# Optimization experiments

Hardware: AMD Instinct MI355X
Metric: run time of the kernel (lower is better)

Reference implementation:

```python
import jax, jax.numpy as jnp
import numpy as np

B, T, D, H = 256, 512, 128, 512

_PARAM_NAMES = [
    "W_i", "U_i", "b_i", "W_i_p", "U_i_p", "b_i_p", "W_i_n", "U_i_n", "b_i_n",
    "W_f", "U_f", "b_f", "W_c", "U_c", "b_c", "W_c_p", "U_c_p", "b_c_p",
    "W_c_n", "U_c_n", "b_c_n", "W_o", "U_o", "b_o", "W_a", "b_a",
]

def _param_shape(name):
    if name == "W_a":
        return (H, H)
    if name.startswith("W"):
        return (D, H)
    if name.startswith("U"):
        return (H, H)
    return (H,)

def setup_inputs() -> dict:
    key = jax.random.key(0)
    keys = jax.random.split(key, len(_PARAM_NAMES) + 3)
    stdv = 1.0 / np.sqrt(H)
    out = {}
    for i, name in enumerate(_PARAM_NAMES):
        out[name] = jax.random.uniform(keys[i], _param_shape(name), jnp.float32, -stdv, stdv)
    out["Y"] = jax.random.normal(keys[-3], (B, T, D), jnp.float32)
    out["P"] = jax.random.normal(keys[-2], (B, T, D), jnp.float32)
    out["N"] = jax.random.normal(keys[-1], (B, T, D), jnp.float32)
    return out


def reference(Y, P, N,
              W_i, U_i, b_i, W_i_p, U_i_p, b_i_p, W_i_n, U_i_n, b_i_n,
              W_f, U_f, b_f, W_c, U_c, b_c, W_c_p, U_c_p, b_c_p,
              W_c_n, U_c_n, b_c_n, W_o, U_o, b_o, W_a, b_a):
    bs = Y.shape[0]
    hid = U_i.shape[0]
    # time-major streams: [T, B, D]
    Yt = jnp.swapaxes(Y, 0, 1)
    Pt = jnp.swapaxes(P, 0, 1)
    Nt = jnp.swapaxes(N, 0, 1)

    sig = jax.nn.sigmoid

    def step(carry, xs):
        h, c = carry
        y_t, p_t, n_t = xs
        i_t = sig(y_t @ W_i + h @ U_i + b_i)
        i_p = sig(p_t @ W_i_p + h @ U_i_p + b_i_p)
        i_n = sig(n_t @ W_i_n + h @ U_i_n + b_i_n)
        f_t = sig(y_t @ W_f + h @ U_f + b_f)
        o_t = sig(y_t @ W_o + h @ U_o + b_o)
        l_t = jnp.tanh(y_t @ W_c + h @ U_c + b_c) * i_t
        l_p = jnp.tanh(p_t @ W_c_p + h @ U_c_p + b_c_p) * i_p
        l_n = jnp.tanh(n_t @ W_c_n + h @ U_c_n + b_c_n) * i_n
        u_t = jnp.tanh((l_t @ W_a) * c + b_a)
        u_p = jnp.tanh((l_p @ W_a) * c + b_a)
        u_n = jnp.tanh((l_n @ W_a) * c + b_a)
        alpha = jax.nn.softmax(jnp.stack([u_t, u_p, u_n]), axis=0)  # [3, B, H]
        L_t = alpha[0] * l_t + alpha[1] * l_p + alpha[2] * l_n
        c_new = f_t * c + L_t
        h_new = o_t * jnp.tanh(c_new)
        return (h_new, c_new), h_new

    h0 = jnp.zeros((bs, hid), Y.dtype)
    c0 = jnp.zeros((bs, hid), Y.dtype)
    (h_last, _), hs = jax.lax.scan(step, (h0, c0), (Yt, Pt, Nt))
    hidden_seq = jnp.swapaxes(hs, 0, 1)  # [B, T, H]
    return h_last, hidden_seq
```

## Files before the change

### kernel.cpp

```cpp
#include <hip/hip_runtime.h>
#include <cstdint>

#define Bb 256
#define Tt 512
#define Dd 128
#define Hh 512
#define BH (Bb*Hh)
#define KGATE 640
#define NCT (Hh/16)
#define MATSZ (KGATE*Hh)
#define LDSB (81920 + 32768 + 3*16*33*4)

typedef unsigned short ushort_t;
typedef __bf16 bf16x8 __attribute__((ext_vector_type(8)));
typedef unsigned short u16x8 __attribute__((ext_vector_type(8)));
typedef float f32x4 __attribute__((ext_vector_type(4)));

static __device__ inline ushort_t f2bf(float f){
    union { float f; uint32_t u; } v; v.f = f;
    uint32_t u = v.u;
    uint32_t r = (u + 0x7FFFu + ((u >> 16) & 1u)) >> 16;
    return (ushort_t)r;
}
static __device__ inline float sigmoidf_(float x){ return 1.f/(1.f+__expf(-x)); }
static __device__ inline float tanhf_(float x){
    float ax = fabsf(x);
    float t = __expf(-2.f*ax);
    float r = (1.f - t)/(1.f + t);
    return copysignf(r, x);
}
static __device__ inline bf16x8 load_x_frag(const float* xp){
    f32x4 v0 = *reinterpret_cast<const f32x4*>(xp);
    f32x4 v1 = *reinterpret_cast<const f32x4*>(xp + 4);
    u16x8 tmp;
    #pragma unroll
    for (int j = 0; j < 4; ++j){ tmp[j] = f2bf(v0[j]); tmp[4+j] = f2bf(v1[j]); }
    return __builtin_bit_cast(bf16x8, tmp);
}

static __device__ inline void st_u32(uint32_t* p, uint32_t v){
    __hip_atomic_store(p, v, __ATOMIC_RELAXED, __HIP_MEMORY_SCOPE_AGENT);
}
static __device__ inline uint32_t ld_u32(const uint32_t* p){
    return __hip_atomic_load(p, __ATOMIC_RELAXED, __HIP_MEMORY_SCOPE_AGENT);
}
static __device__ inline void st_f32(float* p, float v){
    __hip_atomic_store(p, v, __ATOMIC_RELAXED, __HIP_MEMORY_SCOPE_AGENT);
}

__global__ void pack_mat(const float* __restrict__ Wm, const float* __restrict__ Um,
                         int Ktot, ushort_t* __restrict__ dst){
    int total = Ktot * 64;
    for (int g = blockIdx.x*blockDim.x + threadIdx.x; g < total; g += gridDim.x*blockDim.x){
        int kb   = g >> 11;
        int rem  = g & 2047;
        int ct   = rem >> 6;
        int lane = rem & 63;
        int k0   = kb*32 + ((lane >> 4) << 3);
        int col  = (ct << 4) + (lane & 15);
        u16x8 o8;
        #pragma unroll
        for (int j = 0; j < 8; ++j){
            int k = k0 + j;
            float v;
            if (Um) v = (k < Dd) ? Wm[k*Hh + col] : Um[(k - Dd)*Hh + col];
            else    v = Wm[k*Hh + col];
            o8[j] = f2bf(v);
        }
        *reinterpret_cast<u16x8*>(dst + (size_t)g*8) = o8;
    }
}

__global__ void init_state2(ushort_t* hbf, uint32_t* bar){
    int i = blockIdx.x*blockDim.x + threadIdx.x;
    if (i < BH) hbf[i] = 0;
    if (i < 8192) bar[i] = 0;
}

struct PK {
    const ushort_t* wpack;
    const float* X0; const float* X1; const float* X2;
    const float* bC0; const float* bC1; const float* bC2;
    const float* bI0; const float* bI1; const float* bI2;
    const float* bF; const float* bO; const float* b_a;
    ushort_t* hbf;
    ushort_t* l_bf;
    float* l_f;
    float* fo_f;
    uint32_t* bar; float* out;
};

static __device__ inline void group_barrier(uint32_t* gflags, int gb, uint32_t val){
    __builtin_amdgcn_fence(__ATOMIC_RELEASE, "workgroup");
    __syncthreads();
    if (threadIdx.x == 0) st_u32(&gflags[gb*32], val);
    if (threadIdx.x < 64){
        while (ld_u32(&gflags[threadIdx.x*32]) < val)
            __builtin_amdgcn_s_sleep(1);
    }
    __syncthreads();
    __builtin_amdgcn_fence(__ATOMIC_ACQUIRE, "agent");
}

__global__ __launch_bounds__(256, 1) void lstm_persistent(PK A){
    extern __shared__ char lds[];
    ushort_t* Wlds  = (ushort_t*)lds;
    ushort_t* WaLds = (ushort_t*)(lds + 81920);
    float*    u_lds = (float*)(lds + 81920 + 32768);

    const int bid = blockIdx.x;
    const int g   = bid >> 6;
    const int gb  = bid & 63;
    const int tid = threadIdx.x;
    const int lane = tid & 63;
    const int wave = tid >> 6;
    const int r15  = lane & 15;
    const int khi  = (lane >> 4) << 3;
    const int grow0 = g << 6;

    const bool paired = (gb < 48);
    const int s   = gb >> 4;
    const int cs  = gb & 15;
    const int fu  = (gb >= 56) ? 1 : 0;
    const int cfo = (gb - 48) & 7;

    uint32_t* hbf32  = (uint32_t*)A.hbf;
    uint32_t* l_bf32 = (uint32_t*)A.l_bf;

    if (paired){
        const ushort_t* base0 = A.wpack + (size_t)(4 + s)*MATSZ;
        const ushort_t* base1 = A.wpack + (size_t)s*MATSZ;
        for (int u = tid; u < 80*64; u += 256){
            int ch = u >> 6, un = u & 63;
            int m2 = (ch >= 40) ? 1 : 0;
            int rem = ch - m2*40;
            int kb = rem >> 1, j = rem & 1;
            const ushort_t* src = (m2 == 0 ? base0 : base1)
                                + ((size_t)(kb*NCT + cs*2 + j)*64 + un)*8;
            *reinterpret_cast<u16x8*>(Wlds + ((size_t)ch*64 + un)*8)
                = *reinterpret_cast<const u16x8*>(src);
        }
    } else {
        const ushort_t* base = A.wpack + (size_t)(fu == 0 ? 3 : 7)*MATSZ;
        for (int u = tid; u < 80*64; u += 256){
            int ch = u >> 6, un = u & 63;
            int kb = ch >> 2, j = ch & 3;
            const ushort_t* src = base + ((size_t)(kb*NCT + cfo*4 + j)*64 + un)*8;
            *reinterpret_cast<u16x8*>(Wlds + ((size_t)ch*64 + un)*8)
                = *reinterpret_cast<const u16x8*>(src);
        }
    }
    const int rs = gb >> 4, c2 = gb & 15;
    {
        const ushort_t* base = A.wpack + (size_t)8*MATSZ;
        for (int u = tid; u < 32*64; u += 256){
            int ch = u >> 6, un = u & 63;
            int kb = ch >> 1, j = ch & 1;
            const ushort_t* src = base + ((size_t)(kb*NCT + c2*2 + j)*64 + un)*8;
            *reinterpret_cast<u16x8*>(WaLds + ((size_t)ch*64 + un)*8)
                = *reinterpret_cast<const u16x8*>(src);
        }
    }
    __syncthreads();

    float biasA0[4] = {0,0,0,0}, biasA1[2] = {0,0};
    if (paired){
        const float* bCs = (s == 0) ? A.bC0 : (s == 1) ? A.bC1 : A.bC2;
        const float* bIs = (s == 0) ? A.bI0 : (s == 1) ? A.bI1 : A.bI2;
        #pragma unroll
        for (int fj = 0; fj < 2; ++fj){
            int col = cs*32 + fj*16 + r15;
            biasA0[fj] = bCs[col];
            biasA1[fj] = bIs[col];
        }
    } else {
        const float* bb = fu ? A.bO : A.bF;
        #pragma unroll
        for (int fj = 0; fj < 4; ++fj)
            biasA0[fj] = bb[cfo*64 + fj*16 + r15];
    }
    const int rowE = tid >> 5;
    const int colE = tid & 31;
    const int gcol = c2*32 + colE;
    const int growE0 = grow0 + rs*16 + rowE;
    const int growE1 = growE0 + 8;
    const float ba = A.b_a[gcol];
    float creg0 = 0.f, creg1 = 0.f;

    const float* Xs = paired ? ((s == 0) ? A.X0 : (s == 1) ? A.X1 : A.X2) : A.X0;
    uint32_t* gflags = A.bar + g*64*32;
    const int arow = grow0 + wave*16 + r15;

    for (int t = 0; t < Tt; ++t){
        if (paired){
            f32x4 a0[2] = {{0.f,0.f,0.f,0.f},{0.f,0.f,0.f,0.f}};
            f32x4 a1[2] = {{0.f,0.f,0.f,0.f},{0.f,0.f,0.f,0.f}};
            const float* xp = Xs + ((size_t)arow*Tt + t)*Dd + khi;
            #pragma unroll
            for (int kb = 0; kb < KGATE/32; ++kb){
                bf16x8 a;
                if (kb < 4) a = load_x_frag(xp + kb*32);
                else        a = *reinterpret_cast<const bf16x8*>(
                                  A.hbf + (((size_t)(kb-4)*Bb + arow)*32 + khi));
                #pragma unroll
                for (int fj = 0; fj < 2; ++fj){
                    bf16x8 b0 = *reinterpret_cast<const bf16x8*>(Wlds + ((size_t)(kb*2 + fj))*512 + lane*8);
                    a0[fj] = __builtin_amdgcn_mfma_f32_16x16x32_bf16(a, b0, a0[fj], 0, 0, 0);
                    bf16x8 b1 = *reinterpret_cast<const bf16x8*>(Wlds + ((size_t)((20 + kb)*2 + fj))*512 + lane*8);
                    a1[fj] = __builtin_amdgcn_mfma_f32_16x16x32_bf16(a, b1, a1[fj], 0, 0, 0);
                }
            }
            ushort_t* lrep = (ushort_t*)u_lds;
            #pragma unroll
            for (int fj = 0; fj < 2; ++fj)
            #pragma unroll
            for (int r = 0; r < 4; ++r){
                int lrow = wave*16 + ((lane >> 4) << 2) + r;
                int col  = cs*32 + fj*16 + r15;
                size_t idx = (size_t)(grow0 + lrow)*Hh + col;
                float l = tanhf_(a0[fj][r] + biasA0[fj]) * sigmoidf_(a1[fj][r] + biasA1[fj]);
                st_f32(&A.l_f[(size_t)s*BH + idx], l);
                lrep[lrow*32 + fj*16 + r15] = f2bf(l);
            }
            __syncthreads();
            {
                uint32_t* dst = l_bf32 + ((size_t)(s*16 + cs)*Bb + grow0)*16;
                const uint32_t* src = (const uint32_t*)lrep;
                #pragma unroll
                for (int k2 = 0; k2 < 4; ++k2){
                    int idx = tid + k2*256;
                    int lrow = idx >> 4, cp = idx & 15;
                    st_u32(dst + (size_t)lrow*16 + cp, src[idx]);
                }
            }
        } else {
            f32x4 ac[4] = {{0.f,0.f,0.f,0.f},{0.f,0.f,0.f,0.f},{0.f,0.f,0.f,0.f},{0.f,0.f,0.f,0.f}};
            const float* xp = Xs + ((size_t)arow*Tt + t)*Dd + khi;
            #pragma unroll
            for (int kb = 0; kb < KGATE/32; ++kb){
                bf16x8 a;
                if (kb < 4) a = load_x_frag(xp + kb*32);
                else        a = *reinterpret_cast<const bf16x8*>(
                                  A.hbf + (((size_t)(kb-4)*Bb + arow)*32 + khi));
                #pragma unroll
                for (int fj = 0; fj < 4; ++fj){
                    bf16x8 b = *reinterpret_cast<const bf16x8*>(Wlds + ((size_t)(kb*4 + fj))*512 + lane*8);
                    ac[fj] = __builtin_amdgcn_mfma_f32_16x16x32_bf16(a, b, ac[fj], 0, 0, 0);
                }
            }
            #pragma unroll
            for (int fj = 0; fj < 4; ++fj)
            #pragma unroll
            for (int r = 0; r < 4; ++r){
                int lrow = wave*16 + ((lane >> 4) << 2) + r;
                int col  = cfo*64 + fj*16 + r15;
                size_t idx = (size_t)(grow0 + lrow)*Hh + col;
                st_f32(&A.fo_f[(size_t)fu*BH + idx], sigmoidf_(ac[fj][r] + biasA0[fj]));
            }
        }

        group_barrier(gflags, gb, (uint32_t)(2*t + 1));

        if (wave < 3){
            f32x4 acB[2] = {{0.f,0.f,0.f,0.f},{0.f,0.f,0.f,0.f}};
            const int brow = grow0 + rs*16 + r15;
            #pragma unroll
            for (int kb = 0; kb < Hh/32; ++kb){
                bf16x8 a = *reinterpret_cast<const bf16x8*>(
                    A.l_bf + (((size_t)(wave*16 + kb)*Bb + brow)*32 + khi));
                #pragma unroll
                for (int fj = 0; fj < 2; ++fj){
                    bf16x8 b = *reinterpret_cast<const bf16x8*>(WaLds + ((size_t)(kb*2 + fj))*512 + lane*8);
                    acB[fj] = __builtin_amdgcn_mfma_f32_16x16x32_bf16(a, b, acB[fj], 0, 0, 0);
                }
            }
            #pragma unroll
            for (int fj = 0; fj < 2; ++fj)
            #pragma unroll
            for (int r = 0; r < 4; ++r){
                int rowL = ((lane >> 4) << 2) + r;
                int colL = fj*16 + r15;
                u_lds[(wave*16 + rowL)*33 + colL] = acB[fj][r];
            }
        }
        __syncthreads();

        float hn0, hn1;
        {
            #pragma unroll
            for (int e = 0; e < 2; ++e){
                int rowX = rowE + e*8;
                int growX = e ? growE1 : growE0;
                float cv = e ? creg1 : creg0;
                size_t gidx = (size_t)growX*Hh + gcol;
                float u0 = u_lds[(0*16 + rowX)*33 + colE];
                float u1 = u_lds[(1*16 + rowX)*33 + colE];
                float u2 = u_lds[(2*16 + rowX)*33 + colE];
                float e0 = __expf(tanhf_(u0*cv + ba));
                float e1 = __expf(tanhf_(u1*cv + ba));
                float e2 = __expf(tanhf_(u2*cv + ba));
                float inv = 1.f/(e0 + e1 + e2);
                float l0 = A.l_f[gidx];
                float l1 = A.l_f[(size_t)BH + gidx];
                float l2 = A.l_f[(size_t)2*BH + gidx];
                float fg = A.fo_f[gidx];
                float og = A.fo_f[(size_t)BH + gidx];
                float L = (e0*l0 + e1*l1 + e2*l2)*inv;
                float cn = fg*cv + L;
                float hn = og*tanhf_(cn);
                if (e) creg1 = cn; else creg0 = cn;
                __builtin_nontemporal_store(hn, &A.out[(size_t)BH + ((size_t)growX*Tt + t)*Hh + gcol]);
                if (t == Tt - 1) __builtin_nontemporal_store(hn, &A.out[gidx]);
                if (e) hn1 = hn; else hn0 = hn;
            }
        }
        __syncthreads();
        {
            ushort_t* hrep = (ushort_t*)u_lds;
            hrep[rowE*32 + colE]      = f2bf(hn0);
            hrep[(rowE+8)*32 + colE]  = f2bf(hn1);
            __syncthreads();
            uint32_t* dst = hbf32 + ((size_t)c2*Bb + grow0 + rs*16)*16;
            int lr = tid >> 4, cp = tid & 15;
            st_u32(dst + (size_t)lr*16 + cp, ((const uint32_t*)hrep)[tid]);
        }

        if (t != Tt - 1) group_barrier(gflags, gb, (uint32_t)(2*t + 2));
    }
}

extern "C" void kernel_launch(void* const* d_in, const int* in_sizes, int n_in,
                              void* d_out, int out_size, void* d_ws, size_t ws_size,
                              hipStream_t stream){
    const float* in[29];
    for (int i = 0; i < 29; ++i) in[i] = (const float*)d_in[i];

    char* ws = (char*)d_ws;
    ushort_t* wpack = (ushort_t*)(ws + 0);
    ushort_t* hbf   = (ushort_t*)(ws + 5898240);
    ushort_t* l_bf  = (ushort_t*)(ws + 6160384);
    float*    l_f   = (float*)   (ws + 6946816);
    float*    fo_f  = (float*)   (ws + 8519680);
    uint32_t* bar   = (uint32_t*)(ws + 9568256);

    static const int WI[9] = {0, 3, 6, 9, 12, 15, 18, 21, 24};
    static const int UI[9] = {1, 4, 7, 10, 13, 16, 19, 22, -1};
    for (int m = 0; m < 9; ++m){
        int Ktot = (m == 8) ? Hh : KGATE;
        const float* Um = (m == 8) ? nullptr : in[UI[m]];
        int groups = Ktot*64;
        pack_mat<<<dim3((groups + 255)/256), dim3(256), 0, stream>>>(
            in[WI[m]], Um, Ktot, wpack + (size_t)m*MATSZ);
    }
    init_state2<<<dim3(BH/256), dim3(256), 0, stream>>>(hbf, bar);

    PK pk;
    pk.wpack = wpack;
    pk.X0 = in[26]; pk.X1 = in[27]; pk.X2 = in[28];
    pk.bC0 = in[14]; pk.bC1 = in[17]; pk.bC2 = in[20];
    pk.bI0 = in[2];  pk.bI1 = in[5];  pk.bI2 = in[8];
    pk.bF = in[11]; pk.bO = in[23]; pk.b_a = in[25];
    pk.hbf = hbf; pk.l_bf = l_bf; pk.l_f = l_f; pk.fo_f = fo_f;
    pk.bar = bar; pk.out = (float*)d_out;

    hipFuncSetAttribute((const void*)lstm_persistent,
                        hipFuncAttributeMaxDynamicSharedMemorySize, LDSB);
    void* args[] = { &pk };
    hipLaunchCooperativeKernel((const void*)lstm_persistent,
                               dim3(256), dim3(256), args, LDSB, stream);
}
```

Before: 11.86 ms.

## Store gate intermediates in MFMA-fragment layout with 128-bit write-through stores

The l and f/o gate intermediates move to a blocked layout that matches the MFMA accumulator fragments, so each thread writes them with a few 16-byte stores (inline asm with sc0 sc1 cache bits) in place of many scalar relaxed atomic stores. The bf16 l and h exchange buffers are also written with one dwordx4 per thread. The consumer stage recomputes indices into the new layout, and the barrier now waits on vmcnt(0) so the asm stores are complete before signalling. This targets the per-step global store traffic and instruction count on the cross-workgroup exchange path, at the cost of a readback pattern that is less coalesced and reliance on asm cache-policy bits for coherence.

```diff
diff --git a/kernel.cpp b/kernel.cpp
--- a/kernel.cpp
+++ b/kernel.cpp
@@ -15,6 +15,7 @@
 typedef __bf16 bf16x8 __attribute__((ext_vector_type(8)));
 typedef unsigned short u16x8 __attribute__((ext_vector_type(8)));
 typedef float f32x4 __attribute__((ext_vector_type(4)));
+typedef uint32_t u32x4 __attribute__((ext_vector_type(4)));
 
 static __device__ inline ushort_t f2bf(float f){
     union { float f; uint32_t u; } v; v.f = f;
@@ -44,8 +45,8 @@
 static __device__ inline uint32_t ld_u32(const uint32_t* p){
     return __hip_atomic_load(p, __ATOMIC_RELAXED, __HIP_MEMORY_SCOPE_AGENT);
 }
-static __device__ inline void st_f32(float* p, float v){
-    __hip_atomic_store(p, v, __ATOMIC_RELAXED, __HIP_MEMORY_SCOPE_AGENT);
+static __device__ inline void st_wt_x4(void* p, u32x4 d){
+    asm volatile("global_store_dwordx4 %0, %1, off sc0 sc1" :: "v"(p), "v"(d) : "memory");
 }
 
 __global__ void pack_mat(const float* __restrict__ Wm, const float* __restrict__ Um,
@@ -85,12 +86,13 @@
     const float* bF; const float* bO; const float* b_a;
     ushort_t* hbf;
     ushort_t* l_bf;
-    float* l_f;
-    float* fo_f;
+    float* l_f2;
+    float* fo2;
     uint32_t* bar; float* out;
 };
 
 static __device__ inline void group_barrier(uint32_t* gflags, int gb, uint32_t val){
+    asm volatile("s_waitcnt vmcnt(0)" ::: "memory");
     __builtin_amdgcn_fence(__ATOMIC_RELEASE, "workgroup");
     __syncthreads();
     if (threadIdx.x == 0) st_u32(&gflags[gb*32], val);
@@ -116,6 +118,7 @@
     const int wave = tid >> 6;
     const int r15  = lane & 15;
     const int khi  = (lane >> 4) << 3;
+    const int quad = (lane >> 4) << 2;
     const int grow0 = g << 6;
 
     const bool paired = (gb < 48);
@@ -123,9 +126,6 @@
     const int cs  = gb & 15;
     const int fu  = (gb >= 56) ? 1 : 0;
     const int cfo = (gb - 48) & 7;
-
-    uint32_t* hbf32  = (uint32_t*)A.hbf;
-    uint32_t* l_bf32 = (uint32_t*)A.l_bf;
 
     if (paired){
         const ushort_t* base0 = A.wpack + (size_t)(4 + s)*MATSZ;
@@ -188,8 +188,11 @@
     float creg0 = 0.f, creg1 = 0.f;
 
     const float* Xs = paired ? ((s == 0) ? A.X0 : (s == 1) ? A.X1 : A.X2) : A.X0;
-    uint32_t* gflags = A.bar + g*64*32;
+    uint32_t* gflags = A.bar + g*2048;
     const int arow = grow0 + wave*16 + r15;
+
+    float* lf_base = A.l_f2 + (((size_t)(g*3 + s)*16 + cs)*256 + tid)*8;
+    float* fo_base = A.fo2  + (((size_t)(g*2 + fu)*8 + cfo)*256 + tid)*16;
 
     for (int t = 0; t < Tt; ++t){
         if (paired){
@@ -211,27 +214,23 @@
                 }
             }
             ushort_t* lrep = (ushort_t*)u_lds;
+            f32x4 q0, q1;
             #pragma unroll
             for (int fj = 0; fj < 2; ++fj)
             #pragma unroll
             for (int r = 0; r < 4; ++r){
-                int lrow = wave*16 + ((lane >> 4) << 2) + r;
-                int col  = cs*32 + fj*16 + r15;
-                size_t idx = (size_t)(grow0 + lrow)*Hh + col;
+                int lrow = wave*16 + quad + r;
                 float l = tanhf_(a0[fj][r] + biasA0[fj]) * sigmoidf_(a1[fj][r] + biasA1[fj]);
-                st_f32(&A.l_f[(size_t)s*BH + idx], l);
+                if (fj == 0) q0[r] = l; else q1[r] = l;
                 lrep[lrow*32 + fj*16 + r15] = f2bf(l);
             }
+            st_wt_x4(lf_base + 0, __builtin_bit_cast(u32x4, q0));
+            st_wt_x4(lf_base + 4, __builtin_bit_cast(u32x4, q1));
             __syncthreads();
             {
-                uint32_t* dst = l_bf32 + ((size_t)(s*16 + cs)*Bb + grow0)*16;
-                const uint32_t* src = (const uint32_t*)lrep;
-                #pragma unroll
-                for (int k2 = 0; k2 < 4; ++k2){
-                    int idx = tid + k2*256;
-                    int lrow = idx >> 4, cp = idx & 15;
-                    st_u32(dst + (size_t)lrow*16 + cp, src[idx]);
-                }
+                uint32_t* dst = (uint32_t*)A.l_bf + ((size_t)(s*16 + cs)*Bb + grow0)*16;
+                u32x4 d = *reinterpret_cast<const u32x4*>((const uint32_t*)lrep + tid*4);
+                st_wt_x4(dst + tid*4, d);
             }
         } else {
             f32x4 ac[4] = {{0.f,0.f,0.f,0.f},{0.f,0.f,0.f,0.f},{0.f,0.f,0.f,0.f},{0.f,0.f,0.f,0.f}};
@@ -248,15 +247,22 @@
                     ac[fj] = __builtin_amdgcn_mfma_f32_16x16x32_bf16(a, b, ac[fj], 0, 0, 0);
                 }
             }
+            f32x4 qf0, qf1, qf2, qf3;
             #pragma unroll
             for (int fj = 0; fj < 4; ++fj)
             #pragma unroll
             for (int r = 0; r < 4; ++r){
-                int lrow = wave*16 + ((lane >> 4) << 2) + r;
-                int col  = cfo*64 + fj*16 + r15;
-                size_t idx = (size_t)(grow0 + lrow)*Hh + col;
-                st_f32(&A.fo_f[(size_t)fu*BH + idx], sigmoidf_(ac[fj][r] + biasA0[fj]));
-            }
+                float v = sigmoidf_(ac[fj][r] + biasA0[fj]);
+                if      (fj == 0) qf0[r] = v;
+                else if (fj == 1) qf1[r] = v;
+                else if (fj == 2) qf2[r] = v;
+                else              qf3[r] = v;
+            }
+            st_wt_x4(fo_base + 0,  __builtin_bit_cast(u32x4, qf0));
+            st_wt_x4(fo_base + 4,  __builtin_bit_cast(u32x4, qf1));
+            st_wt_x4(fo_base + 8,  __builtin_bit_cast(u32x4, qf2));
+            st_wt_x4(fo_base + 12, __builtin_bit_cast(u32x4, qf3));
+            __syncthreads();
         }
 
         group_barrier(gflags, gb, (uint32_t)(2*t + 1));
@@ -278,9 +284,8 @@
             for (int fj = 0; fj < 2; ++fj)
             #pragma unroll
             for (int r = 0; r < 4; ++r){
-                int rowL = ((lane >> 4) << 2) + r;
-                int colL = fj*16 + r15;
-                u_lds[(wave*16 + rowL)*33 + colL] = acB[fj][r];
+                int rowL = quad + r;
+                u_lds[(wave*16 + rowL)*33 + fj*16 + r15] = acB[fj][r];
             }
         }
         __syncthreads();
@@ -289,28 +294,31 @@
         {
             #pragma unroll
             for (int e = 0; e < 2; ++e){
-                int rowX = rowE + e*8;
+                int q_e = rowE + e*8;
                 int growX = e ? growE1 : growE0;
                 float cv = e ? creg1 : creg0;
-                size_t gidx = (size_t)growX*Hh + gcol;
-                float u0 = u_lds[(0*16 + rowX)*33 + colE];
-                float u1 = u_lds[(1*16 + rowX)*33 + colE];
-                float u2 = u_lds[(2*16 + rowX)*33 + colE];
+                int tidp = rs*64 + ((q_e >> 2) << 4) + (colE & 15);
+                int offl = ((colE >> 4) << 2) + (q_e & 3);
+                int offf = (((gcol >> 4) & 3) << 2) + (q_e & 3);
+                int cfoX = c2 >> 1;
+                float u0 = u_lds[(0*16 + q_e)*33 + colE];
+                float u1 = u_lds[(1*16 + q_e)*33 + colE];
+                float u2 = u_lds[(2*16 + q_e)*33 + colE];
                 float e0 = __expf(tanhf_(u0*cv + ba));
                 float e1 = __expf(tanhf_(u1*cv + ba));
                 float e2 = __expf(tanhf_(u2*cv + ba));
                 float inv = 1.f/(e0 + e1 + e2);
-                float l0 = A.l_f[gidx];
-                float l1 = A.l_f[(size_t)BH + gidx];
-                float l2 = A.l_f[(size_t)2*BH + gidx];
-                float fg = A.fo_f[gidx];
-                float og = A.fo_f[(size_t)BH + gidx];
+                float l0 = A.l_f2[(((size_t)(g*3 + 0)*16 + c2)*256 + tidp)*8 + offl];
+                float l1 = A.l_f2[(((size_t)(g*3 + 1)*16 + c2)*256 + tidp)*8 + offl];
+                float l2 = A.l_f2[(((size_t)(g*3 + 2)*16 + c2)*256 + tidp)*8 + offl];
+                float fg = A.fo2[(((size_t)(g*2 + 0)*8 + cfoX)*256 + tidp)*16 + offf];
+                float og = A.fo2[(((size_t)(g*2 + 1)*8 + cfoX)*256 + tidp)*16 + offf];
                 float L = (e0*l0 + e1*l1 + e2*l2)*inv;
                 float cn = fg*cv + L;
                 float hn = og*tanhf_(cn);
                 if (e) creg1 = cn; else creg0 = cn;
                 __builtin_nontemporal_store(hn, &A.out[(size_t)BH + ((size_t)growX*Tt + t)*Hh + gcol]);
-                if (t == Tt - 1) __builtin_nontemporal_store(hn, &A.out[gidx]);
+                if (t == Tt - 1) __builtin_nontemporal_store(hn, &A.out[(size_t)growX*Hh + gcol]);
                 if (e) hn1 = hn; else hn0 = hn;
             }
         }
@@ -320,9 +328,11 @@
             hrep[rowE*32 + colE]      = f2bf(hn0);
             hrep[(rowE+8)*32 + colE]  = f2bf(hn1);
             __syncthreads();
-            uint32_t* dst = hbf32 + ((size_t)c2*Bb + grow0 + rs*16)*16;
-            int lr = tid >> 4, cp = tid & 15;
-            st_u32(dst + (size_t)lr*16 + cp, ((const uint32_t*)hrep)[tid]);
+            if (tid < 64){
+                uint32_t* dst = (uint32_t*)A.hbf + ((size_t)c2*Bb + grow0 + rs*16)*16;
+                u32x4 d = *reinterpret_cast<const u32x4*>((const uint32_t*)hrep + tid*4);
+                st_wt_x4(dst + tid*4, d);
+            }
         }
 
         if (t != Tt - 1) group_barrier(gflags, gb, (uint32_t)(2*t + 2));
@@ -339,8 +349,8 @@
     ushort_t* wpack = (ushort_t*)(ws + 0);
     ushort_t* hbf   = (ushort_t*)(ws + 5898240);
     ushort_t* l_bf  = (ushort_t*)(ws + 6160384);
-    float*    l_f   = (float*)   (ws + 6946816);
-    float*    fo_f  = (float*)   (ws + 8519680);
+    float*    l_f2  = (float*)   (ws + 6946816);
+    float*    fo2   = (float*)   (ws + 8519680);
     uint32_t* bar   = (uint32_t*)(ws + 9568256);
 
     static const int WI[9] = {0, 3, 6, 9, 12, 15, 18, 21, 24};
@@ -360,7 +370,7 @@
     pk.bC0 = in[14]; pk.bC1 = in[17]; pk.bC2 = in[20];
     pk.bI0 = in[2];  pk.bI1 = in[5];  pk.bI2 = in[8];
     pk.bF = in[11]; pk.bO = in[23]; pk.b_a = in[25];
-    pk.hbf = hbf; pk.l_bf = l_bf; pk.l_f = l_f; pk.fo_f = fo_f;
+    pk.hbf = hbf; pk.l_bf = l_bf; pk.l_f2 = l_f2; pk.fo2 = fo2;
     pk.bar = bar; pk.out = (float*)d_out;
 
     hipFuncSetAttribute((const void*)lstm_persistent,
```

Measured after the change: 12.82 ms. 8.1% more time.

## Switch MFMA operands to fp16 and exchange gate values as packed fp16 tiles

Applied to the files above, without the earlier changes.

Replaces bf16 MFMA with fp16 MFMA throughout, using fp16 for the weights, hidden state and intermediate l values. The per-element fp32 atomic stores of l and f/o gates are dropped. The l values are now read back from the already written fp16 tiled buffer, and the f/o gates are staged through LDS and written as packed 32-bit fp16 tiles. This reduces global traffic and store count in the per-step critical path before the barrier. In exchange it adds extra LDS round-trips and syncs, and uses fp16 storage with lower range for the gate values.

```diff
diff --git a/kernel.cpp b/kernel.cpp
--- a/kernel.cpp
+++ b/kernel.cpp
@@ -12,15 +12,16 @@
 #define LDSB (81920 + 32768 + 3*16*33*4)
 
 typedef unsigned short ushort_t;
-typedef __bf16 bf16x8 __attribute__((ext_vector_type(8)));
+typedef _Float16 h16x8 __attribute__((ext_vector_type(8)));
 typedef unsigned short u16x8 __attribute__((ext_vector_type(8)));
 typedef float f32x4 __attribute__((ext_vector_type(4)));
 
-static __device__ inline ushort_t f2bf(float f){
-    union { float f; uint32_t u; } v; v.f = f;
-    uint32_t u = v.u;
-    uint32_t r = (u + 0x7FFFu + ((u >> 16) & 1u)) >> 16;
-    return (ushort_t)r;
+static __device__ inline ushort_t f2h(float f){
+    _Float16 h = (_Float16)f;
+    return __builtin_bit_cast(ushort_t, h);
+}
+static __device__ inline float h2f(ushort_t u){
+    return (float)__builtin_bit_cast(_Float16, u);
 }
 static __device__ inline float sigmoidf_(float x){ return 1.f/(1.f+__expf(-x)); }
 static __device__ inline float tanhf_(float x){
@@ -29,13 +30,13 @@
     float r = (1.f - t)/(1.f + t);
     return copysignf(r, x);
 }
-static __device__ inline bf16x8 load_x_frag(const float* xp){
+static __device__ inline h16x8 load_x_frag(const float* xp){
     f32x4 v0 = *reinterpret_cast<const f32x4*>(xp);
     f32x4 v1 = *reinterpret_cast<const f32x4*>(xp + 4);
     u16x8 tmp;
     #pragma unroll
-    for (int j = 0; j < 4; ++j){ tmp[j] = f2bf(v0[j]); tmp[4+j] = f2bf(v1[j]); }
-    return __builtin_bit_cast(bf16x8, tmp);
+    for (int j = 0; j < 4; ++j){ tmp[j] = f2h(v0[j]); tmp[4+j] = f2h(v1[j]); }
+    return __builtin_bit_cast(h16x8, tmp);
 }
 
 static __device__ inline void st_u32(uint32_t* p, uint32_t v){
@@ -43,9 +44,6 @@
 }
 static __device__ inline uint32_t ld_u32(const uint32_t* p){
     return __hip_atomic_load(p, __ATOMIC_RELAXED, __HIP_MEMORY_SCOPE_AGENT);
-}
-static __device__ inline void st_f32(float* p, float v){
-    __hip_atomic_store(p, v, __ATOMIC_RELAXED, __HIP_MEMORY_SCOPE_AGENT);
 }
 
 __global__ void pack_mat(const float* __restrict__ Wm, const float* __restrict__ Um,
@@ -65,15 +63,15 @@
             float v;
             if (Um) v = (k < Dd) ? Wm[k*Hh + col] : Um[(k - Dd)*Hh + col];
             else    v = Wm[k*Hh + col];
-            o8[j] = f2bf(v);
+            o8[j] = f2h(v);
         }
         *reinterpret_cast<u16x8*>(dst + (size_t)g*8) = o8;
     }
 }
 
-__global__ void init_state2(ushort_t* hbf, uint32_t* bar){
+__global__ void init_state2(ushort_t* h16, uint32_t* bar){
     int i = blockIdx.x*blockDim.x + threadIdx.x;
-    if (i < BH) hbf[i] = 0;
+    if (i < BH) h16[i] = 0;
     if (i < 8192) bar[i] = 0;
 }
 
@@ -84,9 +82,8 @@
     const float* bI0; const float* bI1; const float* bI2;
     const float* bF; const float* bO; const float* b_a;
     ushort_t* hbf;
-    ushort_t* l_bf;
-    float* l_f;
-    float* fo_f;
+    ushort_t* l16;
+    ushort_t* fo16;
     uint32_t* bar; float* out;
 };
 
@@ -107,6 +104,7 @@
     ushort_t* Wlds  = (ushort_t*)lds;
     ushort_t* WaLds = (ushort_t*)(lds + 81920);
     float*    u_lds = (float*)(lds + 81920 + 32768);
+    ushort_t* srep  = (ushort_t*)u_lds;
 
     const int bid = blockIdx.x;
     const int g   = bid >> 6;
@@ -116,6 +114,7 @@
     const int wave = tid >> 6;
     const int r15  = lane & 15;
     const int khi  = (lane >> 4) << 3;
+    const int quad = (lane >> 4) << 2;
     const int grow0 = g << 6;
 
     const bool paired = (gb < 48);
@@ -123,9 +122,6 @@
     const int cs  = gb & 15;
     const int fu  = (gb >= 56) ? 1 : 0;
     const int cfo = (gb - 48) & 7;
-
-    uint32_t* hbf32  = (uint32_t*)A.hbf;
-    uint32_t* l_bf32 = (uint32_t*)A.l_bf;
 
     if (paired){
         const ushort_t* base0 = A.wpack + (size_t)(4 + s)*MATSZ;
@@ -188,8 +184,11 @@
     float creg0 = 0.f, creg1 = 0.f;
 
     const float* Xs = paired ? ((s == 0) ? A.X0 : (s == 1) ? A.X1 : A.X2) : A.X0;
-    uint32_t* gflags = A.bar + g*64*32;
+    uint32_t* gflags = A.bar + g*2048;
     const int arow = grow0 + wave*16 + r15;
+
+    const int cfoE = gcol >> 6;
+    const int colF = gcol & 63;
 
     for (int t = 0; t < Tt; ++t){
         if (paired){
@@ -198,34 +197,30 @@
             const float* xp = Xs + ((size_t)arow*Tt + t)*Dd + khi;
             #pragma unroll
             for (int kb = 0; kb < KGATE/32; ++kb){
-                bf16x8 a;
+                h16x8 a;
                 if (kb < 4) a = load_x_frag(xp + kb*32);
-                else        a = *reinterpret_cast<const bf16x8*>(
+                else        a = *reinterpret_cast<const h16x8*>(
                                   A.hbf + (((size_t)(kb-4)*Bb + arow)*32 + khi));
                 #pragma unroll
                 for (int fj = 0; fj < 2; ++fj){
-                    bf16x8 b0 = *reinterpret_cast<const bf16x8*>(Wlds + ((size_t)(kb*2 + fj))*512 + lane*8);
-                    a0[fj] = __builtin_amdgcn_mfma_f32_16x16x32_bf16(a, b0, a0[fj], 0, 0, 0);
-                    bf16x8 b1 = *reinterpret_cast<const bf16x8*>(Wlds + ((size_t)((20 + kb)*2 + fj))*512 + lane*8);
-                    a1[fj] = __builtin_amdgcn_mfma_f32_16x16x32_bf16(a, b1, a1[fj], 0, 0, 0);
-                }
-            }
-            ushort_t* lrep = (ushort_t*)u_lds;
+                    h16x8 b0 = *reinterpret_cast<const h16x8*>(Wlds + ((size_t)(kb*2 + fj))*512 + lane*8);
+                    a0[fj] = __builtin_amdgcn_mfma_f32_16x16x32_f16(a, b0, a0[fj], 0, 0, 0);
+                    h16x8 b1 = *reinterpret_cast<const h16x8*>(Wlds + ((size_t)((20 + kb)*2 + fj))*512 + lane*8);
+                    a1[fj] = __builtin_amdgcn_mfma_f32_16x16x32_f16(a, b1, a1[fj], 0, 0, 0);
+                }
+            }
             #pragma unroll
             for (int fj = 0; fj < 2; ++fj)
             #pragma unroll
             for (int r = 0; r < 4; ++r){
-                int lrow = wave*16 + ((lane >> 4) << 2) + r;
-                int col  = cs*32 + fj*16 + r15;
-                size_t idx = (size_t)(grow0 + lrow)*Hh + col;
+                int lrow = wave*16 + quad + r;
                 float l = tanhf_(a0[fj][r] + biasA0[fj]) * sigmoidf_(a1[fj][r] + biasA1[fj]);
-                st_f32(&A.l_f[(size_t)s*BH + idx], l);
-                lrep[lrow*32 + fj*16 + r15] = f2bf(l);
+                srep[lrow*32 + fj*16 + r15] = f2h(l);
             }
             __syncthreads();
             {
-                uint32_t* dst = l_bf32 + ((size_t)(s*16 + cs)*Bb + grow0)*16;
-                const uint32_t* src = (const uint32_t*)lrep;
+                uint32_t* dst = (uint32_t*)A.l16 + ((size_t)(s*16 + cs)*Bb + grow0)*16;
+                const uint32_t* src = (const uint32_t*)srep;
                 #pragma unroll
                 for (int k2 = 0; k2 < 4; ++k2){
                     int idx = tid + k2*256;
@@ -238,24 +233,39 @@
             const float* xp = Xs + ((size_t)arow*Tt + t)*Dd + khi;
             #pragma unroll
             for (int kb = 0; kb < KGATE/32; ++kb){
-                bf16x8 a;
+                h16x8 a;
                 if (kb < 4) a = load_x_frag(xp + kb*32);
-                else        a = *reinterpret_cast<const bf16x8*>(
+                else        a = *reinterpret_cast<const h16x8*>(
                                   A.hbf + (((size_t)(kb-4)*Bb + arow)*32 + khi));
                 #pragma unroll
                 for (int fj = 0; fj < 4; ++fj){
-                    bf16x8 b = *reinterpret_cast<const bf16x8*>(Wlds + ((size_t)(kb*4 + fj))*512 + lane*8);
-                    ac[fj] = __builtin_amdgcn_mfma_f32_16x16x32_bf16(a, b, ac[fj], 0, 0, 0);
-                }
-            }
-            #pragma unroll
-            for (int fj = 0; fj < 4; ++fj)
-            #pragma unroll
-            for (int r = 0; r < 4; ++r){
-                int lrow = wave*16 + ((lane >> 4) << 2) + r;
-                int col  = cfo*64 + fj*16 + r15;
-                size_t idx = (size_t)(grow0 + lrow)*Hh + col;
-                st_f32(&A.fo_f[(size_t)fu*BH + idx], sigmoidf_(ac[fj][r] + biasA0[fj]));
+                    h16x8 b = *reinterpret_cast<const h16x8*>(Wlds + ((size_t)(kb*4 + fj))*512 + lane*8);
+                    ac[fj] = __builtin_amdgcn_mfma_f32_16x16x32_f16(a, b, ac[fj], 0, 0, 0);
+                }
+            }
+            uint32_t* dstc = (uint32_t*)A.fo16 + (size_t)((g*2 + fu)*8 + cfo)*2048;
+            #pragma unroll
+            for (int p = 0; p < 2; ++p){
+                #pragma unroll
+                for (int fj2 = 0; fj2 < 2; ++fj2){
+                    int fj = p*2 + fj2;
+                    #pragma unroll
+                    for (int r = 0; r < 4; ++r){
+                        int lrow = wave*16 + quad + r;
+                        srep[lrow*32 + fj2*16 + r15] = f2h(sigmoidf_(ac[fj][r] + biasA0[fj]));
+                    }
+                }
+                __syncthreads();
+                {
+                    const uint32_t* src = (const uint32_t*)srep;
+                    #pragma unroll
+                    for (int k2 = 0; k2 < 4; ++k2){
+                        int idx = tid + k2*256;
+                        int lrow = idx >> 4, cp = idx & 15;
+                        st_u32(dstc + (size_t)lrow*32 + p*16 + cp, src[idx]);
+                    }
+                }
+                __syncthreads();
             }
         }
 
@@ -266,21 +276,20 @@
             const int brow = grow0 + rs*16 + r15;
             #pragma unroll
             for (int kb = 0; kb < Hh/32; ++kb){
-                bf16x8 a = *reinterpret_cast<const bf16x8*>(
-                    A.l_bf + (((size_t)(wave*16 + kb)*Bb + brow)*32 + khi));
+                h16x8 a = *reinterpret_cast<const h16x8*>(
+                    A.l16 + (((size_t)(wave*16 + kb)*Bb + brow)*32 + khi));
                 #pragma unroll
                 for (int fj = 0; fj < 2; ++fj){
-                    bf16x8 b = *reinterpret_cast<const bf16x8*>(WaLds + ((size_t)(kb*2 + fj))*512 + lane*8);
-                    acB[fj] = __builtin_amdgcn_mfma_f32_16x16x32_bf16(a, b, acB[fj], 0, 0, 0);
+                    h16x8 b = *reinterpret_cast<const h16x8*>(WaLds + ((size_t)(kb*2 + fj))*512 + lane*8);
+                    acB[fj] = __builtin_amdgcn_mfma_f32_16x16x32_f16(a, b, acB[fj], 0, 0, 0);
                 }
             }
             #pragma unroll
             for (int fj = 0; fj < 2; ++fj)
             #pragma unroll
             for (int r = 0; r < 4; ++r){
-                int rowL = ((lane >> 4) << 2) + r;
-                int colL = fj*16 + r15;
-                u_lds[(wave*16 + rowL)*33 + colL] = acB[fj][r];
+                int rowL = quad + r;
+                u_lds[(wave*16 + rowL)*33 + fj*16 + r15] = acB[fj][r];
             }
         }
         __syncthreads();
@@ -292,7 +301,6 @@
                 int rowX = rowE + e*8;
                 int growX = e ? growE1 : growE0;
                 float cv = e ? creg1 : creg0;
-                size_t gidx = (size_t)growX*Hh + gcol;
                 float u0 = u_lds[(0*16 + rowX)*33 + colE];
                 float u1 = u_lds[(1*16 + rowX)*33 + colE];
                 float u2 = u_lds[(2*16 + rowX)*33 + colE];
@@ -300,29 +308,31 @@
                 float e1 = __expf(tanhf_(u1*cv + ba));
                 float e2 = __expf(tanhf_(u2*cv + ba));
                 float inv = 1.f/(e0 + e1 + e2);
-                float l0 = A.l_f[gidx];
-                float l1 = A.l_f[(size_t)BH + gidx];
-                float l2 = A.l_f[(size_t)2*BH + gidx];
-                float fg = A.fo_f[gidx];
-                float og = A.fo_f[(size_t)BH + gidx];
+                size_t lidx = ((size_t)c2*Bb + growX)*32 + colE;
+                float l0 = h2f(A.l16[(size_t)(0*16)*Bb*32 + lidx]);
+                float l1 = h2f(A.l16[(size_t)(1*16)*Bb*32 + lidx]);
+                float l2 = h2f(A.l16[(size_t)(2*16)*Bb*32 + lidx]);
+                size_t fidx = (size_t)((g*2 + 0)*8 + cfoE)*4096 + (size_t)(growX - grow0)*64 + colF;
+                size_t oidx = (size_t)((g*2 + 1)*8 + cfoE)*4096 + (size_t)(growX - grow0)*64 + colF;
+                float fg = h2f(A.fo16[fidx]);
+                float og = h2f(A.fo16[oidx]);
                 float L = (e0*l0 + e1*l1 + e2*l2)*inv;
                 float cn = fg*cv + L;
                 float hn = og*tanhf_(cn);
                 if (e) creg1 = cn; else creg0 = cn;
                 __builtin_nontemporal_store(hn, &A.out[(size_t)BH + ((size_t)growX*Tt + t)*Hh + gcol]);
-                if (t == Tt - 1) __builtin_nontemporal_store(hn, &A.out[gidx]);
+                if (t == Tt - 1) __builtin_nontemporal_store(hn, &A.out[(size_t)growX*Hh + gcol]);
                 if (e) hn1 = hn; else hn0 = hn;
             }
         }
         __syncthreads();
         {
-            ushort_t* hrep = (ushort_t*)u_lds;
-            hrep[rowE*32 + colE]      = f2bf(hn0);
-            hrep[(rowE+8)*32 + colE]  = f2bf(hn1);
+            srep[rowE*32 + colE]      = f2h(hn0);
+            srep[(rowE+8)*32 + colE]  = f2h(hn1);
             __syncthreads();
-            uint32_t* dst = hbf32 + ((size_t)c2*Bb + grow0 + rs*16)*16;
+            uint32_t* dst = (uint32_t*)A.hbf + ((size_t)c2*Bb + grow0 + rs*16)*16;
             int lr = tid >> 4, cp = tid & 15;
-            st_u32(dst + (size_t)lr*16 + cp, ((const uint32_t*)hrep)[tid]);
+            st_u32(dst + (size_t)lr*16 + cp, ((const uint32_t*)srep)[tid]);
         }
 
         if (t != Tt - 1) group_barrier(gflags, gb, (uint32_t)(2*t + 2));
@@ -337,11 +347,10 @@
 
     char* ws = (char*)d_ws;
     ushort_t* wpack = (ushort_t*)(ws + 0);
-    ushort_t* hbf   = (ushort_t*)(ws + 5898240);
-    ushort_t* l_bf  = (ushort_t*)(ws + 6160384);
-    float*    l_f   = (float*)   (ws + 6946816);
-    float*    fo_f  = (float*)   (ws + 8519680);
-    uint32_t* bar   = (uint32_t*)(ws + 9568256);
+    ushort_t* h16   = (ushort_t*)(ws + 5898240);
+    ushort_t* l16   = (ushort_t*)(ws + 6160384);
+    ushort_t* fo16  = (ushort_t*)(ws + 6946816);
+    uint32_t* bar   = (uint32_t*)(ws + 7471104);
 
     static const int WI[9] = {0, 3, 6, 9, 12, 15, 18, 21, 24};
     static const int UI[9] = {1, 4, 7, 10, 13, 16, 19, 22, -1};
@@ -352,7 +361,7 @@
         pack_mat<<<dim3((groups + 255)/256), dim3(256), 0, stream>>>(
             in[WI[m]], Um, Ktot, wpack + (size_t)m*MATSZ);
     }
-    init_state2<<<dim3(BH/256), dim3(256), 0, stream>>>(hbf, bar);
+    init_state2<<<dim3(BH/256), dim3(256), 0, stream>>>(h16, bar);
 
     PK pk;
     pk.wpack = wpack;
@@ -360,7 +369,7 @@
     pk.bC0 = in[14]; pk.bC1 = in[17]; pk.bC2 = in[20];
     pk.bI0 = in[2];  pk.bI1 = in[5];  pk.bI2 = in[8];
     pk.bF = in[11]; pk.bO = in[23]; pk.b_a = in[25];
-    pk.hbf = hbf; pk.l_bf = l_bf; pk.l_f = l_f; pk.fo_f = fo_f;
+    pk.hbf = h16; pk.l16 = l16; pk.fo16 = fo16;
     pk.bar = bar; pk.out = (float*)d_out;
 
     hipFuncSetAttribute((const void*)lstm_persistent,
```

Result: no change. 11.82 ms (-0.4%).
